# Performance work log

Hardware: AMD Instinct MI355X
Metric: run time of the kernel (lower is better)

## Reference

```python
import jax, jax.numpy as jnp
import numpy as np

BETA = 0.1
PAD = 0
NORMALIZE_LENGTH = True
B, T, V = 64, 512, 512


def setup_inputs() -> dict:
    key = jax.random.key(0)
    k1, k2, k3, k4 = jax.random.split(key, 4)
    inp = jax.random.normal(k1, (B, T, V), dtype=jnp.float32)
    target = jax.random.randint(k2, (B, T), 0, V, dtype=jnp.int64 if jax.config.read('jax_enable_x64') else jnp.int32)
    length = jax.random.randint(k3, (B,), 1, T).astype(jnp.float32)
    # confusion matrix: rows over last axis normalized to sum to 1 (probabilities)
    m = jax.random.uniform(k4, (V, V, V), dtype=jnp.float32)
    matric = m / m.sum(axis=-1, keepdims=True)
    return {"input": inp, "target": target, "length": length, "matric": matric}


def reference(input, target, length, matric):
    b, t, v = input.shape
    n = b * t
    # previous-token targets (shifted right, first position = 0)
    forth = jnp.concatenate([jnp.zeros((b, 1), target.dtype), target[:, :-1]], axis=1).reshape(-1)
    tgt = target.reshape(-1)
    ignore = tgt == PAD                     # [N]
    total = ignore.sum().astype(input.dtype)
    log_prob = jax.nn.log_softmax(input.reshape(n, v), axis=-1)  # [N, V]
    # per-utterance smoothing 1 - (1-beta)^(1/L), broadcast over time
    smoothing = 1.0 - jnp.power(1.0 - BETA, 1.0 / length)        # [B]
    smoothing = jnp.broadcast_to(smoothing[:, None], (b, t)).reshape(-1)  # [N]
    # gather V-length confusion rows indexed by (prev, cur) token pair
    weight = smoothing[:, None] * matric[forth, tgt, :]          # [N, V]
    src = 1.0 - weight.sum(axis=1)                               # [N]
    weight = weight.at[jnp.arange(n), tgt].set(src)              # scatter diag mass
    denom = total if NORMALIZE_LENGTH else jnp.asarray(b, input.dtype)
    loss = jnp.where(ignore[:, None], 0.0, -weight * log_prob).sum() / denom
    return loss
```

## Files before the change

kernel.cpp:

```cpp
#include <hip/hip_runtime.h>


#define T_DIM 512
#define V_DIM 512
#define LN_0_9 (-0.1053605157f)

__device__ __forceinline__ float pick4(float4 v, int k) {
    const float lo = (k & 1) ? v.y : v.x;
    const float hi = (k & 1) ? v.w : v.z;
    return (k & 2) ? hi : lo;
}

__global__ __launch_bounds__(256) void pwl_main_kernel(
    const float* __restrict__ input,
    const int*   __restrict__ target,
    const float* __restrict__ length,
    const float* __restrict__ matric,
    float*       __restrict__ ws,
    int N, int nwaves)
{
    const int lane = threadIdx.x & 63;
    const int wave = threadIdx.x >> 6;
    const int wgid = blockIdx.x * 4 + wave;

    int ts[4], fs[4];
    #pragma unroll
    for (int p = 0; p < 4; ++p) {
        const int n = wgid + p * nwaves;
        if (n < N) {
            ts[p] = target[n];
            const int tp = n & (T_DIM - 1);
            fs[p] = (tp == 0) ? 0 : target[n - 1];
        } else {
            ts[p] = -1;
            fs[p] = 0;
        }
    }

    float acc_sum = 0.0f;
    int   acc_cnt = 0;

    #pragma unroll
    for (int p = 0; p < 4; ++p) {
        const int n = wgid + p * nwaves;
        const int t = ts[p];
        if (t < 0) continue;
        if (t == 0) { acc_cnt++; continue; }

        const int b = n / T_DIM;
        const int f = fs[p];

        const float4* xrow = (const float4*)(input + (size_t)n * V_DIM);
        const float4 x0 = xrow[lane];
        const float4 x1 = xrow[lane + 64];

        const float4* mrow = (const float4*)(matric + ((size_t)f * V_DIM + t) * V_DIM);
        const float4 m0 = mrow[lane];
        const float4 m1 = mrow[lane + 64];

        float mx = fmaxf(fmaxf(fmaxf(x0.x, x0.y), fmaxf(x0.z, x0.w)),
                         fmaxf(fmaxf(x1.x, x1.y), fmaxf(x1.z, x1.w)));
        #pragma unroll
        for (int off = 32; off > 0; off >>= 1)
            mx = fmaxf(mx, __shfl_xor(mx, off, 64));

        float se = expf(x0.x - mx) + expf(x0.y - mx) + expf(x0.z - mx) + expf(x0.w - mx)
                 + expf(x1.x - mx) + expf(x1.y - mx) + expf(x1.z - mx) + expf(x1.w - mx);
        #pragma unroll
        for (int off = 32; off > 0; off >>= 1)
            se += __shfl_xor(se, off, 64);
        const float lse = mx + logf(se);

        float dot = m0.x * x0.x + m0.y * x0.y + m0.z * x0.z + m0.w * x0.w
                  + m1.x * x1.x + m1.y * x1.y + m1.z * x1.z + m1.w * x1.w;
        float rs  = m0.x + m0.y + m0.z + m0.w + m1.x + m1.y + m1.z + m1.w;
        #pragma unroll
        for (int off = 32; off > 0; off >>= 1) {
            dot += __shfl_xor(dot, off, 64);
            rs  += __shfl_xor(rs,  off, 64);
        }

        const int  k       = t & 3;
        const int  srcLane = (t >> 2) & 63;
        const bool hiHalf  = (t >= 256);
        const float cm = hiHalf ? pick4(m1, k) : pick4(m0, k);
        const float cx = hiHalf ? pick4(x1, k) : pick4(x0, k);
        const float Mt = __shfl(cm, srcLane, 64);
        const float xt = __shfl(cx, srcLane, 64);

        const float L = length[b];
        const float s = 1.0f - expf(LN_0_9 / L);
        const float src = 1.0f - s * rs;
        const float contrib = s * (dot - lse * rs) + (src - s * Mt) * (xt - lse);
        acc_sum += contrib;
    }

    if (lane == 0) {
        ws[wgid]          = acc_sum;
        ws[nwaves + wgid] = (float)acc_cnt;
    }
}

__global__ __launch_bounds__(256) void pwl_final_kernel(
    const float* __restrict__ ws, float* __restrict__ out, int nwaves)
{
    const int lane = threadIdx.x & 63;
    const int wave = threadIdx.x >> 6;

    float s = 0.0f, c = 0.0f;
    for (int i = threadIdx.x; i < nwaves; i += 256) {
        s += ws[i];
        c += ws[nwaves + i];
    }
    #pragma unroll
    for (int off = 32; off > 0; off >>= 1) {
        s += __shfl_xor(s, off, 64);
        c += __shfl_xor(c, off, 64);
    }

    __shared__ float ss[4], sc[4];
    if (lane == 0) { ss[wave] = s; sc[wave] = c; }
    __syncthreads();
    if (threadIdx.x == 0) {
        float S = ss[0] + ss[1] + ss[2] + ss[3];
        float C = sc[0] + sc[1] + sc[2] + sc[3];
        out[0] = -S / C;
    }
}

extern "C" void kernel_launch(void* const* d_in, const int* in_sizes, int n_in,
                              void* d_out, int out_size, void* d_ws, size_t ws_size,
                              hipStream_t stream) {
    const float* input  = (const float*)d_in[0];
    const int*   target = (const int*)  d_in[1];
    const float* length = (const float*)d_in[2];
    const float* matric = (const float*)d_in[3];
    float* out = (float*)d_out;
    float* ws  = (float*)d_ws;

    const int N = in_sizes[1];

    const int blocks = (N + 15) / 16;
    const int nwaves = blocks * 4;

    pwl_main_kernel<<<blocks, 256, 0, stream>>>(input, target, length, matric, ws, N, nwaves);
    pwl_final_kernel<<<1, 256, 0, stream>>>(ws, out, nwaves);
}
```

Baseline: 630.2 us.

## Batch two rows per wave with all loads issued upfront, block-level partial reduce

Each wave now handles two rows instead of four, and issues all input and matrix loads for both rows before any arithmetic, so the memory requests are in flight together. The grid doubles in size, and the per-wave partial sums are combined in shared memory so only one value per block goes to the workspace. Loads are now issued even for padding-target rows (using a clamped index), which adds some unneeded traffic in exchange for uniform, overlapped memory access.

```diff
diff --git a/kernel.cpp b/kernel.cpp
--- a/kernel.cpp
+++ b/kernel.cpp
@@ -17,100 +17,119 @@
     const float* __restrict__ length,
     const float* __restrict__ matric,
     float*       __restrict__ ws,
-    int N, int nwaves)
+    int N, int nwp)
 {
     const int lane = threadIdx.x & 63;
     const int wave = threadIdx.x >> 6;
     const int wgid = blockIdx.x * 4 + wave;
 
-    int ts[4], fs[4];
+    int n[2] = { wgid, wgid + nwp };
+    int t[2], f[2];
     #pragma unroll
-    for (int p = 0; p < 4; ++p) {
-        const int n = wgid + p * nwaves;
-        if (n < N) {
-            ts[p] = target[n];
-            const int tp = n & (T_DIM - 1);
-            fs[p] = (tp == 0) ? 0 : target[n - 1];
+    for (int p = 0; p < 2; ++p) {
+        if (n[p] < N) {
+            t[p] = target[n[p]];
+            f[p] = ((n[p] & (T_DIM - 1)) == 0) ? 0 : target[n[p] - 1];
         } else {
-            ts[p] = -1;
-            fs[p] = 0;
+            t[p] = -1;
+            f[p] = 0;
+            n[p] = 0;
         }
+    }
+
+    float4 x0[2], x1[2], m0[2], m1[2];
+    #pragma unroll
+    for (int p = 0; p < 2; ++p) {
+        const float4* xrow = (const float4*)(input + (size_t)n[p] * V_DIM);
+        x0[p] = xrow[lane];
+        x1[p] = xrow[lane + 64];
+        const int tc = (t[p] > 0) ? t[p] : 0;
+        const float4* mrow = (const float4*)(matric + ((size_t)f[p] * V_DIM + tc) * V_DIM);
+        m0[p] = mrow[lane];
+        m1[p] = mrow[lane + 64];
+    }
+
+    float mx[2];
+    #pragma unroll
+    for (int p = 0; p < 2; ++p)
+        mx[p] = fmaxf(fmaxf(fmaxf(x0[p].x, x0[p].y), fmaxf(x0[p].z, x0[p].w)),
+                      fmaxf(fmaxf(x1[p].x, x1[p].y), fmaxf(x1[p].z, x1[p].w)));
+    #pragma unroll
+    for (int off = 32; off > 0; off >>= 1) {
+        mx[0] = fmaxf(mx[0], __shfl_xor(mx[0], off, 64));
+        mx[1] = fmaxf(mx[1], __shfl_xor(mx[1], off, 64));
+    }
+
+    float se[2];
+    #pragma unroll
+    for (int p = 0; p < 2; ++p)
+        se[p] = expf(x0[p].x - mx[p]) + expf(x0[p].y - mx[p])
+              + expf(x0[p].z - mx[p]) + expf(x0[p].w - mx[p])
+              + expf(x1[p].x - mx[p]) + expf(x1[p].y - mx[p])
+              + expf(x1[p].z - mx[p]) + expf(x1[p].w - mx[p]);
+    #pragma unroll
+    for (int off = 32; off > 0; off >>= 1) {
+        se[0] += __shfl_xor(se[0], off, 64);
+        se[1] += __shfl_xor(se[1], off, 64);
+    }
+
+    float dot[2], rs[2];
+    #pragma unroll
+    for (int p = 0; p < 2; ++p) {
+        dot[p] = m0[p].x * x0[p].x + m0[p].y * x0[p].y + m0[p].z * x0[p].z + m0[p].w * x0[p].w
+               + m1[p].x * x1[p].x + m1[p].y * x1[p].y + m1[p].z * x1[p].z + m1[p].w * x1[p].w;
+        rs[p]  = m0[p].x + m0[p].y + m0[p].z + m0[p].w
+               + m1[p].x + m1[p].y + m1[p].z + m1[p].w;
+    }
+    #pragma unroll
+    for (int off = 32; off > 0; off >>= 1) {
+        dot[0] += __shfl_xor(dot[0], off, 64);
+        dot[1] += __shfl_xor(dot[1], off, 64);
+        rs[0]  += __shfl_xor(rs[0],  off, 64);
+        rs[1]  += __shfl_xor(rs[1],  off, 64);
     }
 
     float acc_sum = 0.0f;
     int   acc_cnt = 0;
+    #pragma unroll
+    for (int p = 0; p < 2; ++p) {
+        if (t[p] < 0) continue;
+        if (t[p] == 0) { acc_cnt++; continue; }
+        const float lse = mx[p] + logf(se[p]);
 
-    #pragma unroll
-    for (int p = 0; p < 4; ++p) {
-        const int n = wgid + p * nwaves;
-        const int t = ts[p];
-        if (t < 0) continue;
-        if (t == 0) { acc_cnt++; continue; }
-
-        const int b = n / T_DIM;
-        const int f = fs[p];
-
-        const float4* xrow = (const float4*)(input + (size_t)n * V_DIM);
-        const float4 x0 = xrow[lane];
-        const float4 x1 = xrow[lane + 64];
-
-        const float4* mrow = (const float4*)(matric + ((size_t)f * V_DIM + t) * V_DIM);
-        const float4 m0 = mrow[lane];
-        const float4 m1 = mrow[lane + 64];
-
-        float mx = fmaxf(fmaxf(fmaxf(x0.x, x0.y), fmaxf(x0.z, x0.w)),
-                         fmaxf(fmaxf(x1.x, x1.y), fmaxf(x1.z, x1.w)));
-        #pragma unroll
-        for (int off = 32; off > 0; off >>= 1)
-            mx = fmaxf(mx, __shfl_xor(mx, off, 64));
-
-        float se = expf(x0.x - mx) + expf(x0.y - mx) + expf(x0.z - mx) + expf(x0.w - mx)
-                 + expf(x1.x - mx) + expf(x1.y - mx) + expf(x1.z - mx) + expf(x1.w - mx);
-        #pragma unroll
-        for (int off = 32; off > 0; off >>= 1)
-            se += __shfl_xor(se, off, 64);
-        const float lse = mx + logf(se);
-
-        float dot = m0.x * x0.x + m0.y * x0.y + m0.z * x0.z + m0.w * x0.w
-                  + m1.x * x1.x + m1.y * x1.y + m1.z * x1.z + m1.w * x1.w;
-        float rs  = m0.x + m0.y + m0.z + m0.w + m1.x + m1.y + m1.z + m1.w;
-        #pragma unroll
-        for (int off = 32; off > 0; off >>= 1) {
-            dot += __shfl_xor(dot, off, 64);
-            rs  += __shfl_xor(rs,  off, 64);
-        }
-
-        const int  k       = t & 3;
-        const int  srcLane = (t >> 2) & 63;
-        const bool hiHalf  = (t >= 256);
-        const float cm = hiHalf ? pick4(m1, k) : pick4(m0, k);
-        const float cx = hiHalf ? pick4(x1, k) : pick4(x0, k);
+        const int  k       = t[p] & 3;
+        const int  srcLane = (t[p] >> 2) & 63;
+        const bool hiHalf  = (t[p] >= 256);
+        const float cm = hiHalf ? pick4(m1[p], k) : pick4(m0[p], k);
+        const float cx = hiHalf ? pick4(x1[p], k) : pick4(x0[p], k);
         const float Mt = __shfl(cm, srcLane, 64);
         const float xt = __shfl(cx, srcLane, 64);
 
-        const float L = length[b];
+        const float L = length[n[p] >> 9];
         const float s = 1.0f - expf(LN_0_9 / L);
-        const float src = 1.0f - s * rs;
-        const float contrib = s * (dot - lse * rs) + (src - s * Mt) * (xt - lse);
-        acc_sum += contrib;
+        const float src = 1.0f - s * rs[p];
+        acc_sum += s * (dot[p] - lse * rs[p]) + (src - s * Mt) * (xt - lse);
     }
 
-    if (lane == 0) {
-        ws[wgid]          = acc_sum;
-        ws[nwaves + wgid] = (float)acc_cnt;
+    __shared__ float ss[4], sc[4];
+    if (lane == 0) { ss[wave] = acc_sum; sc[wave] = (float)acc_cnt; }
+    __syncthreads();
+    if (threadIdx.x == 0) {
+        ws[blockIdx.x]             = ss[0] + ss[1] + ss[2] + ss[3];
+        ws[gridDim.x + blockIdx.x] = sc[0] + sc[1] + sc[2] + sc[3];
     }
 }
 
 __global__ __launch_bounds__(256) void pwl_final_kernel(
-    const float* __restrict__ ws, float* __restrict__ out, int nwaves)
+    const float* __restrict__ ws, float* __restrict__ out, int nb)
 {
     const int lane = threadIdx.x & 63;
     const int wave = threadIdx.x >> 6;
 
     float s = 0.0f, c = 0.0f;
-    for (int i = threadIdx.x; i < nwaves; i += 256) {
+    for (int i = threadIdx.x; i < nb; i += 256) {
         s += ws[i];
-        c += ws[nwaves + i];
+        c += ws[nb + i];
     }
     #pragma unroll
     for (int off = 32; off > 0; off >>= 1) {
@@ -122,8 +141,8 @@
     if (lane == 0) { ss[wave] = s; sc[wave] = c; }
     __syncthreads();
     if (threadIdx.x == 0) {
-        float S = ss[0] + ss[1] + ss[2] + ss[3];
-        float C = sc[0] + sc[1] + sc[2] + sc[3];
+        const float S = ss[0] + ss[1] + ss[2] + ss[3];
+        const float C = sc[0] + sc[1] + sc[2] + sc[3];
         out[0] = -S / C;
     }
 }
@@ -140,9 +159,9 @@
 
     const int N = in_sizes[1];
 
-    const int blocks = (N + 15) / 16;
-    const int nwaves = blocks * 4;
+    const int blocks = (N + 7) / 8;
+    const int nwp    = blocks * 4;
 
-    pwl_main_kernel<<<blocks, 256, 0, stream>>>(input, target, length, matric, ws, N, nwaves);
-    pwl_final_kernel<<<1, 256, 0, stream>>>(ws, out, nwaves);
+    pwl_main_kernel<<<blocks, 256, 0, stream>>>(input, target, length, matric, ws, N, nwp);
+    pwl_final_kernel<<<1, 256, 0, stream>>>(ws, out, blocks);
 }
```

Result: no change. 624.3 us (-0.9%).
